# Kernel tuning notes

Measured on AMD Instinct MI355X. Metric: run time of the kernel, lower is better.

Reference implementation:

```python
import jax, jax.numpy as jnp
import numpy as np

B, V, S = 64, 8, 32        # batch, n_views, volume scale
N = 2 * S                  # graph nodes: 2 stacked views x 32 slices
F = S * S                  # node features: flattened 32x32 slice
EPS = 1e-5                 # BatchNorm eps
NEG = -9e15                # SemGraphConv mask value


def setup_inputs() -> dict:
    key = jax.random.key(0)
    ks = jax.random.split(key, 32)
    x = jax.random.normal(ks[0], (B, V, S, S, S), dtype=jnp.float32)
    # derangement over views (original rejects any idx with a fixed point)
    idx = jnp.roll(jnp.arange(V, dtype=jnp.int32), 1)

    def adj_mask(k):
        m = jax.random.bernoulli(k, 0.15, (N, N))
        return (m | jnp.eye(N, dtype=bool)).astype(jnp.int32)

    d = {"x": x, "idx": idx, "adj1": adj_mask(ks[1]), "adj2": adj_mask(ks[2])}
    for c, k0 in zip((1, 2, 3), (3, 10, 17)):
        d[f"W{c}"] = (jax.random.normal(ks[k0], (2, F, F)) * 0.02).astype(jnp.float32)
        d[f"e{c}"] = (jax.random.normal(ks[k0 + 1], (N, N)) * 0.1).astype(jnp.float32)
        d[f"b{c}"] = jnp.zeros((F,), jnp.float32)
        d[f"gamma{c}"] = jnp.ones((F,), jnp.float32)
        d[f"beta{c}"] = jnp.zeros((F,), jnp.float32)
        d[f"rmean{c}"] = jnp.zeros((F,), jnp.float32)
        d[f"rvar{c}"] = jnp.ones((F,), jnp.float32)
    return d


def _sem_gconv(x, W, e, bias, mask):
    # x: [Bv, N, F]; W: [2, F, F]; e, mask: [N, N]
    h0 = jnp.einsum('bnf,fg->bng', x, W[0])
    h1 = jnp.einsum('bnf,fg->bng', x, W[1])
    logits = jnp.where(mask > 0, e, NEG)
    A = jax.nn.softmax(logits, axis=1)
    diag = jnp.diagonal(A)                      # A * I @ h0 == diag(A) * h0
    A_off = A * (1.0 - jnp.eye(N, dtype=A.dtype))
    out = diag[None, :, None] * h0 + jnp.einsum('nm,bmg->bng', A_off, h1)
    return out + bias


def _gblock(x, W, e, b, gamma, beta, rmean, rvar, mask):
    h = _sem_gconv(x, W, e, b, mask)
    # BatchNorm1d over the feature/channel dim (inference form), then ReLU
    h = (h - rmean) * (gamma * jax.lax.rsqrt(rvar + EPS)) + beta
    return jax.nn.relu(h)


def _channel(x, idx, perm_in, perm_out, params, mask):
    xp = jnp.transpose(x, perm_in)                      # [B,V,S,S,S]
    pairs = jnp.stack([xp, xp[:, idx]], axis=2)         # [B,V,2,S,S,S]
    nodes = pairs.reshape(B * V, N, F)                  # [B*V, 64, 1024]
    h = _gblock(nodes, *params, mask)
    h = h.reshape(B, V, 2, S, S, S).mean(axis=2)        # mean over the pair
    return jnp.transpose(h, perm_out)


def reference(x, idx, adj1, adj2,
              W1, e1, b1, gamma1, beta1, rmean1, rvar1,
              W2, e2, b2, gamma2, beta2, rmean2, rvar2,
              W3, e3, b3, gamma3, beta3, rmean3, rvar3):
    p1 = (W1, e1, b1, gamma1, beta1, rmean1, rvar1)
    p2 = (W2, e2, b2, gamma2, beta2, rmean2, rvar2)
    p3 = (W3, e3, b3, gamma3, beta3, rmean3, rvar3)
    c1 = _channel(x, idx, (0, 1, 4, 2, 3), (0, 1, 3, 4, 2), p1, adj1)
    c2 = _channel(x, idx, (0, 1, 2, 3, 4), (0, 1, 2, 3, 4), p2, adj2)
    c3 = _channel(x, idx, (0, 1, 3, 2, 4), (0, 1, 3, 2, 4), p3, adj2)
    return 0.5 * c1 + 0.25 * c2 + 0.25 * c3
```

## Files before the change

kernel.cpp:

```cpp
#include <hip/hip_runtime.h>
#include <stdint.h>

typedef __attribute__((ext_vector_type(8))) short short8;
typedef __attribute__((ext_vector_type(16))) float f32x16;
typedef __attribute__((ext_vector_type(4))) unsigned short ushort4v;

union S8 { short8 v; unsigned short u[8]; };

static __device__ __forceinline__ unsigned short f2bf(float f) {
  union { float f; unsigned u; } v; v.f = f;
  unsigned r = v.u + 0x7fffu + ((v.u >> 16) & 1u);
  return (unsigned short)(r >> 16);
}
static __device__ __forceinline__ float bf2f(unsigned short u) {
  union { unsigned u; float f; } v; v.u = ((unsigned)u) << 16;
  return v.f;
}

static __device__ __forceinline__ void glds16(const void* g, void* l) {
  __builtin_amdgcn_global_load_lds(
      (const __attribute__((address_space(1))) unsigned int*)g,
      (__attribute__((address_space(3))) unsigned int*)l, 16, 0, 0);
}

__global__ __launch_bounds__(256) void prep_w(const float* __restrict__ Wa,
                                              const float* __restrict__ Wb,
                                              const float* __restrict__ Wc,
                                              unsigned short* __restrict__ wfrag) {
  int t    = blockIdx.x * 256 + threadIdx.x;
  int lane = t & 63;
  int tt   = (t >> 6) & 7;
  int ks   = (t >> 9) & 1;
  int kt   = (t >> 10) & 31;
  int g8   = (t >> 15) & 7;
  int c    = t >> 18;
  const float* W = (c == 0) ? Wa : (c == 1) ? Wb : Wc;
  int s  = tt >> 2, gt = tt & 3;
  int g  = g8*128 + gt*32 + (lane & 31);
  int k0 = kt*32 + ks*16 + ((lane >> 5) * 8);
  const float* src = W + (size_t)s * 1048576 + (size_t)k0 * 1024 + g;
  unsigned short* dst = wfrag + (size_t)t * 8;
#pragma unroll
  for (int e = 0; e < 8; ++e) dst[e] = f2bf(src[(size_t)e * 1024]);
}

__global__ __launch_bounds__(256) void prep_x2(const float* __restrict__ x,
                                               int c, unsigned short* __restrict__ ximg) {
  int t = blockIdx.x * 256 + threadIdx.x;
  int lane = t & 63;
  int ks = (t >> 6) & 1;
  int kt = (t >> 7) & 31;
  int vid = t >> 12;
  const float* src = x + (size_t)vid * 32768;
  int i = lane & 31;
  int k0 = kt*32 + ks*16 + ((lane >> 5) * 8);
  S8 pk;
  if (c == 0) {
#pragma unroll
    for (int e = 0; e < 8; ++e) pk.u[e] = f2bf(src[(size_t)(k0 + e)*32 + i]);
  } else {
    const float* sp = (c == 1) ? (src + i*1024 + k0)
                               : (src + (k0 >> 5)*1024 + i*32 + (k0 & 31));
    float4 u0 = *(const float4*)sp, u1 = *(const float4*)(sp + 4);
    pk.u[0]=f2bf(u0.x); pk.u[1]=f2bf(u0.y); pk.u[2]=f2bf(u0.z); pk.u[3]=f2bf(u0.w);
    pk.u[4]=f2bf(u1.x); pk.u[5]=f2bf(u1.y); pk.u[6]=f2bf(u1.z); pk.u[7]=f2bf(u1.w);
  }
  *(short8*)(ximg + (size_t)t * 8) = pk.v;
}

__global__ __launch_bounds__(256) void prep_misc(
    const float* e0, const int* a0, const float* b0, const float* g0, const float* be0, const float* rm0, const float* rv0,
    const float* e1, const int* a1, const float* b1, const float* g1, const float* be1, const float* rm1, const float* rv1,
    const float* e2, const int* a2, const float* b2, const float* g2, const float* be2, const float* rm2, const float* rv2,
    unsigned short* __restrict__ aofrag, float* __restrict__ diagA,
    float* __restrict__ scale2, float* __restrict__ shift2) {
  __shared__ float A[64][64];
  int c = blockIdx.x;
  int tid = threadIdx.x;
  const float* ev = (c==0)?e0:(c==1)?e1:e2;
  const int*   ad = (c==0)?a0:(c==1)?a1:a2;
  const float* bb = (c==0)?b0:(c==1)?b1:b2;
  const float* gm = (c==0)?g0:(c==1)?g1:g2;
  const float* bt = (c==0)?be0:(c==1)?be1:be2;
  const float* rm = (c==0)?rm0:(c==1)?rm1:rm2;
  const float* rv = (c==0)?rv0:(c==1)?rv1:rv2;
  if (tid < 64) {
    int n = tid;
    float mx = -3.0e38f;
    for (int m = 0; m < 64; ++m) {
      float lg = (ad[n*64+m] > 0) ? ev[n*64+m] : -9.0e15f;
      A[n][m] = lg; mx = fmaxf(mx, lg);
    }
    float ssum = 0.f;
    for (int m = 0; m < 64; ++m) { float p = __expf(A[n][m] - mx); A[n][m] = p; ssum += p; }
    float inv = 1.f / ssum;
    for (int m = 0; m < 64; ++m) A[n][m] *= inv;
  }
  __syncthreads();
  if (tid < 64) diagA[c*64 + tid] = A[tid][tid];
  for (int idx = tid; idx < 4096; idx += 256) {
    int e  = idx & 7;
    int l  = (idx >> 3) & 63;
    int ks = (idx >> 9) & 3;
    int nt = idx >> 11;
    int n = nt*32 + (l & 31);
    int m = ks*16 + ((l >> 5) * 8) + e;
    float vv = (m == n) ? 0.f : A[n][m];
    aofrag[c*4096 + idx] = f2bf(vv);
  }
  for (int g = tid; g < 1024; g += 256) {
    float sc = gm[g] * rsqrtf(rv[g] + 1e-5f);
    scale2[c*1024 + g] = sc;
    shift2[c*1024 + g] = bt[g] + (bb[g] - rm[g]) * sc;
  }
}

template<int CH>
__device__ __forceinline__ void loadAfb(float av[2][8], const float* __restrict__ sview,
                                        int d0, int lh, int kt) {
#pragma unroll
  for (int ks = 0; ks < 2; ++ks) {
    int kb = kt*32 + ks*16 + lh*8;
    if (CH == 0) {
#pragma unroll
      for (int e = 0; e < 8; ++e) av[ks][e] = sview[(size_t)(kb + e)*32 + d0];
    } else if (CH == 1) {
      const float* sp = sview + d0*1024 + kb;
      *(float4*)&av[ks][0] = *(const float4*)sp;
      *(float4*)&av[ks][4] = *(const float4*)(sp + 4);
    } else {
      const float* sp = sview + kt*1024 + d0*32 + ks*16 + lh*8;
      *(float4*)&av[ks][0] = *(const float4*)sp;
      *(float4*)&av[ks][4] = *(const float4*)(sp + 4);
    }
  }
}

template<int CH, int IMG>
__global__ __launch_bounds__(512, 2) void gconv(
    const float* __restrict__ x, const int* __restrict__ idxp,
    const unsigned short* __restrict__ wimg, const unsigned short* __restrict__ ximg,
    const unsigned short* __restrict__ aofrag,
    const float* __restrict__ diagA, const float* __restrict__ scale2,
    const float* __restrict__ shift2, float* __restrict__ out) {
  __shared__ alignas(128) char lds[131072];
  int tid = threadIdx.x, lane = tid & 63, wave = tid >> 6;
  int l31 = lane & 31, lh = lane >> 5;
  int wm = wave >> 1, sn = wave & 1;
  int bid = blockIdx.x;
  int g8 = bid & 7, b = bid >> 3;
  int v0l = 2*wm, v1l = v0l + 1;
  size_t vid0 = (size_t)b*8 + v0l, vid1 = vid0 + 1;
  const float* xv0 = x + vid0 * 32768;
  const float* xv1 = x + vid1 * 32768;

  const char* srcB  = (const char*)wimg + (size_t)g8 * 524288 + tid*16;
  const char* srcA0 = (const char*)ximg + vid0 * 65536 + lane*16;
  const char* srcA1 = (const char*)ximg + vid1 * 65536 + lane*16;

  f32x16 acc[2][4];
#pragma unroll
  for (int mt = 0; mt < 2; ++mt)
#pragma unroll
    for (int gt = 0; gt < 4; ++gt)
#pragma unroll
      for (int r = 0; r < 16; ++r) acc[mt][gt][r] = 0.f;

  char* pB0 = lds;  char* pB1 = lds + 16384;  char* pB2 = lds + 32768;
  int dW = wave * 1024;

  auto stageB = [&](char* dst, int kt) {
    const char* s = srcB + (size_t)kt * 16384;
    glds16(s,        dst + dW);
    glds16(s + 8192, dst + dW + 8192);
  };
  auto loadAreg = [&](short8 a[4], int kt) {
    if (IMG) {
      const char* s0 = srcA0 + (size_t)kt * 2048;
      const char* s1 = srcA1 + (size_t)kt * 2048;
      a[0] = *(const short8*)s0;
      a[1] = *(const short8*)s1;
      a[2] = *(const short8*)(s0 + 1024);
      a[3] = *(const short8*)(s1 + 1024);
    } else {
#pragma unroll
      for (int h = 0; h < 2; ++h) {
        alignas(16) float av[2][8];
        loadAfb<CH>(av, h ? xv1 : xv0, l31, lh, kt);
#pragma unroll
        for (int ks = 0; ks < 2; ++ks) {
          S8 pk;
#pragma unroll
          for (int e = 0; e < 8; ++e) pk.u[e] = f2bf(av[ks][e]);
          a[ks*2 + h] = pk.v;
        }
      }
    }
  };
  auto compute = [&](const char* bB, const short8 a[4]) {
    __builtin_amdgcn_s_setprio(1);
#pragma unroll
    for (int ks = 0; ks < 2; ++ks) {
      const char* bp = bB + ((ks*8 + sn*4)*64 + lane)*16;
#pragma unroll
      for (int gt = 0; gt < 4; ++gt) {
        short8 bf = *(const short8*)(bp + gt*1024);
        acc[0][gt] = __builtin_amdgcn_mfma_f32_32x32x16_bf16(a[ks*2    ], bf, acc[0][gt], 0, 0, 0);
        acc[1][gt] = __builtin_amdgcn_mfma_f32_32x32x16_bf16(a[ks*2 + 1], bf, acc[1][gt], 0, 0, 0);
      }
    }
    __builtin_amdgcn_s_setprio(0);
  };
  auto waitk = [&]() {
    if (IMG) asm volatile("s_waitcnt vmcnt(2)" ::: "memory");
    else     asm volatile("s_waitcnt vmcnt(0) lgkmcnt(0)" ::: "memory");
    __builtin_amdgcn_s_barrier();
  };

  short8 aE[4], aN[4];

  loadAreg(aE, 0);
  __builtin_amdgcn_sched_barrier(0);
  stageB(pB0, 0);
  __builtin_amdgcn_sched_barrier(0);
  stageB(pB1, 1);
  __builtin_amdgcn_sched_barrier(0);

#pragma unroll 1
  for (int kt = 0; kt < 30; kt += 2) {
    waitk();
    loadAreg(aN, kt + 1);
    __builtin_amdgcn_sched_barrier(0);
    stageB(pB2, kt + 2);
    __builtin_amdgcn_sched_barrier(0);
    compute(pB0, aE);
    { char* t = pB0; pB0 = pB1; pB1 = pB2; pB2 = t; }
    waitk();
    loadAreg(aE, kt + 2);
    __builtin_amdgcn_sched_barrier(0);
    stageB(pB2, kt + 3);
    __builtin_amdgcn_sched_barrier(0);
    compute(pB0, aN);
    { char* t = pB0; pB0 = pB1; pB1 = pB2; pB2 = t; }
  }
  waitk();
  loadAreg(aN, 31);
  __builtin_amdgcn_sched_barrier(0);
  compute(pB0, aE);
  { char* t = pB0; pB0 = pB1; pB1 = pB2; pB2 = t; }
  asm volatile("s_waitcnt vmcnt(0) lgkmcnt(0)" ::: "memory");
  __builtin_amdgcn_s_barrier();
  compute(pB0, aN);
  __syncthreads();

  char* H1r = lds;
  char* H0r = lds + 65536;
  if (sn == 1) {
#pragma unroll
    for (int mt = 0; mt < 2; ++mt) {
      int vloc = v0l + mt;
#pragma unroll
      for (int gt = 0; gt < 4; ++gt) {
        int col = gt*32 + l31;
        int xw = (col & 3) << 4;
        char* cb = H1r + vloc*8192 + col*64;
#pragma unroll
        for (int j = 0; j < 4; ++j) {
          ushort4v pk;
          pk.x = f2bf(acc[mt][gt][4*j+0]);
          pk.y = f2bf(acc[mt][gt][4*j+1]);
          pk.z = f2bf(acc[mt][gt][4*j+2]);
          pk.w = f2bf(acc[mt][gt][4*j+3]);
          *(ushort4v*)(cb + ((j*16 + lh*8) ^ xw)) = pk;
        }
      }
    }
  } else {
#pragma unroll
    for (int mt = 0; mt < 2; ++mt) {
      int vloc = v0l + mt;
#pragma unroll
      for (int gt = 0; gt < 4; ++gt) {
        char* cb = H0r + vloc*8192 + gt*2048 + lane*16;
        S8 lo, hi;
#pragma unroll
        for (int e = 0; e < 8; ++e) { lo.u[e] = f2bf(acc[mt][gt][e]); hi.u[e] = f2bf(acc[mt][gt][8+e]); }
        *(short8*)cb = lo.v;
        *(short8*)(cb + 1024) = hi.v;
      }
    }
  }
  __syncthreads();

  {
    int v = wave;
    int v2 = idxp[v];
    f32x16 agg[2][4];
#pragma unroll
    for (int nt = 0; nt < 2; ++nt)
#pragma unroll
      for (int gt = 0; gt < 4; ++gt)
#pragma unroll
        for (int r = 0; r < 16; ++r) agg[nt][gt][r] = 0.f;

#pragma unroll
    for (int ks = 0; ks < 4; ++ks) {
      int vsel = (ks < 2) ? v : v2;
      int ksl = ks & 1;
      short8 aof0 = *(const short8*)((const char*)aofrag + (size_t)((0*4 + ks)*64 + lane)*16);
      short8 aof1 = *(const short8*)((const char*)aofrag + (size_t)((1*4 + ks)*64 + lane)*16);
#pragma unroll
      for (int gt = 0; gt < 4; ++gt) {
        int col = gt*32 + l31;
        int xw = (col & 3) << 4;
        short8 hf = *(const short8*)(H1r + vsel*8192 + col*64 + ((ksl*32 + lh*16) ^ xw));
        agg[0][gt] = __builtin_amdgcn_mfma_f32_32x32x16_bf16(aof0, hf, agg[0][gt], 0, 0, 0);
        agg[1][gt] = __builtin_amdgcn_mfma_f32_32x32x16_bf16(aof1, hf, agg[1][gt], 0, 0, 0);
      }
    }

    size_t gid = (size_t)b*8 + v;
    size_t obase = gid * 32768;
#pragma unroll
    for (int gt = 0; gt < 4; ++gt) {
      int g = g8*128 + gt*32 + l31;
      float sc = scale2[g], sh = shift2[g];
      S8 h0a0, h0a1, h0b0, h0b1;
      h0a0.v = *(const short8*)(H0r + v *8192 + gt*2048 + lane*16);
      h0a1.v = *(const short8*)(H0r + v *8192 + gt*2048 + 1024 + lane*16);
      h0b0.v = *(const short8*)(H0r + v2*8192 + gt*2048 + lane*16);
      h0b1.v = *(const short8*)(H0r + v2*8192 + gt*2048 + 1024 + lane*16);
#pragma unroll
      for (int j = 0; j < 4; ++j) {
        int i00 = j*8 + lh*4;
        float res[4];
#pragma unroll
        for (int jj = 0; jj < 4; ++jj) {
          int q = j*4 + jj;
          int i = i00 + jj;
          float h0v  = (q < 8) ? bf2f(h0a0.u[q]) : bf2f(h0a1.u[q-8]);
          float h0v2 = (q < 8) ? bf2f(h0b0.u[q]) : bf2f(h0b1.u[q-8]);
          float va = diagA[i]      * h0v  + agg[0][gt][q];
          float vb = diagA[32 + i] * h0v2 + agg[1][gt][q];
          va = fmaxf(va * sc + sh, 0.f);
          vb = fmaxf(vb * sc + sh, 0.f);
          res[jj] = 0.5f * (va + vb);
        }
        if (CH == 0) {
          float4 o4;
          o4.x = 0.5f*res[0]; o4.y = 0.5f*res[1]; o4.z = 0.5f*res[2]; o4.w = 0.5f*res[3];
          *(float4*)(out + obase + (size_t)g*32 + i00) = o4;
        } else if (CH == 1) {
#pragma unroll
          for (int jj = 0; jj < 4; ++jj)
            out[obase + (size_t)(i00 + jj)*1024 + g] += 0.25f * res[jj];
        } else {
#pragma unroll
          for (int jj = 0; jj < 4; ++jj)
            out[obase + (size_t)(g >> 5)*1024 + (size_t)(i00 + jj)*32 + (g & 31)] += 0.25f * res[jj];
        }
      }
    }
  }
}

extern "C" void kernel_launch(void* const* d_in, const int* in_sizes, int n_in,
                              void* d_out, int out_size, void* d_ws, size_t ws_size,
                              hipStream_t stream) {
  (void)in_sizes; (void)n_in; (void)out_size;
  const float* x    = (const float*)d_in[0];
  const int*   idx  = (const int*)d_in[1];
  const int*   adj1 = (const int*)d_in[2];
  const int*   adj2 = (const int*)d_in[3];
  const float *W[3], *e[3], *bb[3], *gm[3], *bt[3], *rm[3], *rv[3];
  for (int c = 0; c < 3; ++c) {
    int base = 4 + c*7;
    W[c]  = (const float*)d_in[base + 0];
    e[c]  = (const float*)d_in[base + 1];
    bb[c] = (const float*)d_in[base + 2];
    gm[c] = (const float*)d_in[base + 3];
    bt[c] = (const float*)d_in[base + 4];
    rm[c] = (const float*)d_in[base + 5];
    rv[c] = (const float*)d_in[base + 6];
  }
  char* ws = (char*)d_ws;
  unsigned short* wfrag  = (unsigned short*)ws;
  unsigned short* aofrag = (unsigned short*)(ws + 12582912);
  float* diagA  = (float*)(ws + 12607488);
  float* scale2 = (float*)(ws + 12608256);
  float* shift2 = (float*)(ws + 12620544);
  unsigned short* ximg = (unsigned short*)(ws + 16777216);
  bool img = ws_size >= (size_t)(16777216 + 33554432);

  prep_w<<<3072, 256, 0, stream>>>(W[0], W[1], W[2], wfrag);
  prep_misc<<<3, 256, 0, stream>>>(
      e[0], adj1, bb[0], gm[0], bt[0], rm[0], rv[0],
      e[1], adj2, bb[1], gm[1], bt[1], rm[1], rv[1],
      e[2], adj2, bb[2], gm[2], bt[2], rm[2], rv[2],
      aofrag, diagA, scale2, shift2);

  float* out = (float*)d_out;
  if (img) {
    prep_x2<<<8192, 256, 0, stream>>>(x, 0, ximg);
    gconv<0,1><<<512, 512, 0, stream>>>(x, idx, wfrag, ximg, aofrag,
                                        diagA, scale2, shift2, out);
    prep_x2<<<8192, 256, 0, stream>>>(x, 1, ximg);
    gconv<1,1><<<512, 512, 0, stream>>>(x, idx, wfrag + 2097152, ximg, aofrag + 4096,
                                        diagA + 64,  scale2 + 1024, shift2 + 1024, out);
    prep_x2<<<8192, 256, 0, stream>>>(x, 2, ximg);
    gconv<2,1><<<512, 512, 0, stream>>>(x, idx, wfrag + 4194304, ximg, aofrag + 8192,
                                        diagA + 128, scale2 + 2048, shift2 + 2048, out);
  } else {
    gconv<0,0><<<512, 512, 0, stream>>>(x, idx, wfrag, ximg, aofrag,
                                        diagA, scale2, shift2, out);
    gconv<1,0><<<512, 512, 0, stream>>>(x, idx, wfrag + 2097152, ximg, aofrag + 4096,
                                        diagA + 64,  scale2 + 1024, shift2 + 1024, out);
    gconv<2,0><<<512, 512, 0, stream>>>(x, idx, wfrag + 4194304, ximg, aofrag + 8192,
                                        diagA + 128, scale2 + 2048, shift2 + 2048, out);
  }
}
```

Baseline: 362.4 us.

## Load weight fragments directly into registers instead of staging through LDS

Drops the triple-buffered LDS staging of weight tiles with global_load_lds and the per-step barriers. Each wave now loads its own B fragments from global memory into registers, double-buffered alongside the A fragments. Launch bounds move to one block per SM so more registers are available. The aim is to remove barrier and LDS traffic, at the cost of duplicated global loads across the four wave-rows that share a weight tile, and lower occupancy.

```diff
diff --git a/kernel.cpp b/kernel.cpp
--- a/kernel.cpp
+++ b/kernel.cpp
@@ -15,12 +15,6 @@
 static __device__ __forceinline__ float bf2f(unsigned short u) {
   union { unsigned u; float f; } v; v.u = ((unsigned)u) << 16;
   return v.f;
-}
-
-static __device__ __forceinline__ void glds16(const void* g, void* l) {
-  __builtin_amdgcn_global_load_lds(
-      (const __attribute__((address_space(1))) unsigned int*)g,
-      (__attribute__((address_space(3))) unsigned int*)l, 16, 0, 0);
 }
 
 __global__ __launch_bounds__(256) void prep_w(const float* __restrict__ Wa,
@@ -137,7 +131,7 @@
 }
 
 template<int CH, int IMG>
-__global__ __launch_bounds__(512, 2) void gconv(
+__global__ __launch_bounds__(512, 1) void gconv(
     const float* __restrict__ x, const int* __restrict__ idxp,
     const unsigned short* __restrict__ wimg, const unsigned short* __restrict__ ximg,
     const unsigned short* __restrict__ aofrag,
@@ -154,7 +148,7 @@
   const float* xv0 = x + vid0 * 32768;
   const float* xv1 = x + vid1 * 32768;
 
-  const char* srcB  = (const char*)wimg + (size_t)g8 * 524288 + tid*16;
+  const char* srcB  = (const char*)wimg + (size_t)g8 * 524288 + sn*4096 + lane*16;
   const char* srcA0 = (const char*)ximg + vid0 * 65536 + lane*16;
   const char* srcA1 = (const char*)ximg + vid1 * 65536 + lane*16;
 
@@ -166,13 +160,13 @@
 #pragma unroll
       for (int r = 0; r < 16; ++r) acc[mt][gt][r] = 0.f;
 
-  char* pB0 = lds;  char* pB1 = lds + 16384;  char* pB2 = lds + 32768;
-  int dW = wave * 1024;
-
-  auto stageB = [&](char* dst, int kt) {
+  auto loadB = [&](short8 bfr[8], int kt) {
     const char* s = srcB + (size_t)kt * 16384;
-    glds16(s,        dst + dW);
-    glds16(s + 8192, dst + dW + 8192);
+#pragma unroll
+    for (int ks = 0; ks < 2; ++ks)
+#pragma unroll
+      for (int gt = 0; gt < 4; ++gt)
+        bfr[ks*4 + gt] = *(const short8*)(s + ks*8192 + gt*1024);
   };
   auto loadAreg = [&](short8 a[4], int kt) {
     if (IMG) {
@@ -197,61 +191,42 @@
       }
     }
   };
-  auto compute = [&](const char* bB, const short8 a[4]) {
+  auto computeR = [&](const short8 a[4], const short8 bfr[8]) {
     __builtin_amdgcn_s_setprio(1);
 #pragma unroll
-    for (int ks = 0; ks < 2; ++ks) {
-      const char* bp = bB + ((ks*8 + sn*4)*64 + lane)*16;
+    for (int ks = 0; ks < 2; ++ks)
 #pragma unroll
       for (int gt = 0; gt < 4; ++gt) {
-        short8 bf = *(const short8*)(bp + gt*1024);
-        acc[0][gt] = __builtin_amdgcn_mfma_f32_32x32x16_bf16(a[ks*2    ], bf, acc[0][gt], 0, 0, 0);
-        acc[1][gt] = __builtin_amdgcn_mfma_f32_32x32x16_bf16(a[ks*2 + 1], bf, acc[1][gt], 0, 0, 0);
-      }
-    }
+        acc[0][gt] = __builtin_amdgcn_mfma_f32_32x32x16_bf16(a[ks*2    ], bfr[ks*4+gt], acc[0][gt], 0, 0, 0);
+        acc[1][gt] = __builtin_amdgcn_mfma_f32_32x32x16_bf16(a[ks*2 + 1], bfr[ks*4+gt], acc[1][gt], 0, 0, 0);
+      }
     __builtin_amdgcn_s_setprio(0);
   };
-  auto waitk = [&]() {
-    if (IMG) asm volatile("s_waitcnt vmcnt(2)" ::: "memory");
-    else     asm volatile("s_waitcnt vmcnt(0) lgkmcnt(0)" ::: "memory");
-    __builtin_amdgcn_s_barrier();
-  };
-
-  short8 aE[4], aN[4];
+
+  short8 aE[4], aN[4], bE[8], bN[8];
 
   loadAreg(aE, 0);
-  __builtin_amdgcn_sched_barrier(0);
-  stageB(pB0, 0);
-  __builtin_amdgcn_sched_barrier(0);
-  stageB(pB1, 1);
-  __builtin_amdgcn_sched_barrier(0);
+  loadB(bE, 0);
+  loadAreg(aN, 1);
+  loadB(bN, 1);
 
 #pragma unroll 1
-  for (int kt = 0; kt < 30; kt += 2) {
-    waitk();
-    loadAreg(aN, kt + 1);
-    __builtin_amdgcn_sched_barrier(0);
-    stageB(pB2, kt + 2);
-    __builtin_amdgcn_sched_barrier(0);
-    compute(pB0, aE);
-    { char* t = pB0; pB0 = pB1; pB1 = pB2; pB2 = t; }
-    waitk();
+  for (int kt = 0; kt < 28; kt += 2) {
+    computeR(aE, bE);
     loadAreg(aE, kt + 2);
-    __builtin_amdgcn_sched_barrier(0);
-    stageB(pB2, kt + 3);
-    __builtin_amdgcn_sched_barrier(0);
-    compute(pB0, aN);
-    { char* t = pB0; pB0 = pB1; pB1 = pB2; pB2 = t; }
-  }
-  waitk();
+    loadB(bE, kt + 2);
+    computeR(aN, bN);
+    loadAreg(aN, kt + 3);
+    loadB(bN, kt + 3);
+  }
+  computeR(aE, bE);
+  loadAreg(aE, 30);
+  loadB(bE, 30);
+  computeR(aN, bN);
   loadAreg(aN, 31);
-  __builtin_amdgcn_sched_barrier(0);
-  compute(pB0, aE);
-  { char* t = pB0; pB0 = pB1; pB1 = pB2; pB2 = t; }
-  asm volatile("s_waitcnt vmcnt(0) lgkmcnt(0)" ::: "memory");
-  __builtin_amdgcn_s_barrier();
-  compute(pB0, aN);
-  __syncthreads();
+  loadB(bN, 31);
+  computeR(aE, bE);
+  computeR(aN, bN);
 
   char* H1r = lds;
   char* H0r = lds + 65536;
```

New measurement: 368.1 us. No clear change (+1.6%).
